# Kernel optimization log

Measured on AMD Instinct MI355X. Metric: run time of the kernel, lower is better.

The kernel has to match this reference:

```python
import jax, jax.numpy as jnp
import numpy as np

H = 1024   # dim_hidden
K = 64     # number of tasks
T_STEPS = 2048


def setup_inputs() -> dict:
    key = jax.random.key(0)
    ks = jax.random.split(key, 12)
    s = 1.0 / np.sqrt(H)
    inp = {
        "z":    jax.random.normal(ks[0], (H,), jnp.float32),
        "Wih":  jax.random.normal(ks[1], (4 * H, H), jnp.float32) * s,
        "Whh":  jax.random.normal(ks[2], (4 * H, H), jnp.float32) * s,
        "b_ih": jax.random.normal(ks[3], (4 * H,), jnp.float32) * s,
        "b_hh": jax.random.normal(ks[4], (4 * H,), jnp.float32) * s,
        "W1":   jax.random.normal(ks[5], (32, H), jnp.float32) * s,
        "b1":   jax.random.normal(ks[6], (32,), jnp.float32) * s,
        "W2":   jax.random.normal(ks[7], (32, 32), jnp.float32) * (1.0 / np.sqrt(32)),
        "b2":   jax.random.normal(ks[8], (32,), jnp.float32) * (1.0 / np.sqrt(32)),
        "W3":   jax.random.normal(ks[9], (K, 32), jnp.float32) * (1.0 / np.sqrt(32)),
        "b3":   jax.random.normal(ks[10], (K,), jnp.float32) * (1.0 / np.sqrt(32)),
        "T":    T_STEPS,
    }
    return inp


def reference(z, Wih, Whh, b_ih, b_hh, W1, b1, W2, b2, W3, b3, T):
    h0 = jnp.zeros_like(z)
    c0 = jnp.zeros_like(z)

    def cell(carry, _):
        x, h, c = carry  # x is the LSTM input this step (z first, then fed-back h)
        gates = x @ Wih.T + b_ih + h @ Whh.T + b_hh  # (4H,), torch gate order i,f,g,o
        i, f, g, o = jnp.split(gates, 4)
        c_new = jax.nn.sigmoid(f) * c + jax.nn.sigmoid(i) * jnp.tanh(g)
        h_new = jax.nn.sigmoid(o) * jnp.tanh(c_new)
        # torch LSTM output y == h_new; fed back as next input
        return (h_new, h_new, c_new), h_new

    _, hs = jax.lax.scan(cell, (z, h0, c0), None, length=T)  # hs: (T, H)

    # MLP applied per timestep, vectorized over T
    a = jax.nn.relu(hs @ W1.T + b1)
    a = jax.nn.relu(a @ W2.T + b2)
    rewards = a @ W3.T + b3  # (T, K)
    return rewards
```

## Files before the change

kernel.cpp:

```cpp
#include <hip/hip_runtime.h>
#include <math.h>

#define H        1024
#define TSTEPS   2048
#define NWG      64
#define NT       1024
#define PAD      68
#define SENT     0xFFFFFFFFu

typedef unsigned u32x4 __attribute__((ext_vector_type(4)));
typedef float    f32x2 __attribute__((ext_vector_type(2)));
typedef float    f32x4 __attribute__((ext_vector_type(4)));
typedef unsigned long long u64;

__device__ __forceinline__ u32x4 load16_agent(const unsigned* p) {
    u32x4 r;
    asm volatile("global_load_dwordx4 %0, %1, off sc1\n\ts_waitcnt vmcnt(0)"
                 : "=v"(r) : "v"(p) : "memory");
    return r;
}

__device__ __forceinline__ u64 load8_agent(const unsigned* p) {
    u64 r;
    asm volatile("global_load_dwordx2 %0, %1, off sc1\n\ts_waitcnt vmcnt(0)"
                 : "=v"(r) : "v"(p) : "memory");
    return r;
}

__device__ __forceinline__ void pkfma(f32x2& acc, f32x2 a, f32x2 b) {
    asm("v_pk_fma_f32 %0, %1, %2, %0" : "+v"(acc) : "v"(a), "v"(b));
}

__device__ __forceinline__ float fsig(float x)   { return 1.0f / (1.0f + __expf(-x)); }
__device__ __forceinline__ float ftanh_(float x) { return 1.0f - 2.0f / (__expf(2.0f * x) + 1.0f); }

__global__ __launch_bounds__(NT, 1) void lstm_persistent(
    const float* __restrict__ z,   const float* __restrict__ Wih,
    const float* __restrict__ Whh, const float* __restrict__ b_ih,
    const float* __restrict__ b_hh,
    const float* __restrict__ W1,  const float* __restrict__ b1,
    const float* __restrict__ W2,  const float* __restrict__ b2,
    const float* __restrict__ W3,  const float* __restrict__ b3,
    float* __restrict__ out, float* __restrict__ hs)
{
    __shared__ __align__(16) float hbuf[2][16 * PAD];
    __shared__ unsigned h_out[2][16];
    __shared__ __align__(16) float mlp_buf[4][16 * PAD];
    __shared__ float a1_lds[4][32];
    __shared__ float a2_lds[4][32];

    const int tid  = threadIdx.x;
    const int wg   = blockIdx.x;
    const int wave = tid >> 6;
    const int lane = tid & 63;
    const int g    = lane >> 4;
    const int seg  = lane & 15;
    const int E    = wg * 16 + wave;
    const int grow = g * H + E;
    const float bias = b_ih[grow] + b_hh[grow];

    if (tid < 32) h_out[tid >> 4][tid & 15] = SENT;

    if (tid < 256) {
        float4 zv = *(const float4*)(z + tid * 4);
        *(float4*)(&hbuf[0][(tid >> 4) * PAD + (tid & 15) * 4]) = zv;
    }
    __syncthreads();

    f32x4 wreg[16];
    float s0 = 0.f, s1 = 0.f, s2 = 0.f, s3 = 0.f;
    const float* wihp = Wih + (size_t)grow * H + seg * 64;
    const float* whhp = Whh + (size_t)grow * H + seg * 64;
#pragma unroll
    for (int k = 0; k < 16; ++k) {
        f32x4 a  = *(const f32x4*)(wihp + 4 * k);
        f32x4 b  = *(const f32x4*)(whhp + 4 * k);
        f32x4 zz = *(const f32x4*)(&hbuf[0][seg * PAD + 4 * k]);
        float d = a.x * zz.x + a.y * zz.y + a.z * zz.z + a.w * zz.w;
        if ((k & 3) == 0) s0 += d; else if ((k & 3) == 1) s1 += d;
        else if ((k & 3) == 2) s2 += d; else s3 += d;
        wreg[k] = a + b;
    }
    float c_reg;
    {
        float acc = (s0 + s1) + (s2 + s3);
        acc += __shfl_xor(acc, 1); acc += __shfl_xor(acc, 2);
        acc += __shfl_xor(acc, 4); acc += __shfl_xor(acc, 8);
        float val = acc + bias;
        float act = (g == 2) ? ftanh_(val) : fsig(val);
        float si = __shfl(act, 0), tg = __shfl(act, 32), so = __shfl(act, 48);
        c_reg = si * tg;
        float hn = so * ftanh_(c_reg);
        if (lane == 0) ((volatile unsigned*)h_out[0])[wave] = __float_as_uint(hn);
        if (wave == 15) {
            unsigned v;
            do { v = ((volatile unsigned*)h_out[0])[lane & 15]; } while (!__all(v != SENT));
            if (lane < 16) {
                __hip_atomic_store((unsigned*)hs + wg * 16 + lane, v,
                                   __ATOMIC_RELAXED, __HIP_MEMORY_SCOPE_AGENT);
                ((volatile unsigned*)h_out[0])[lane] = SENT;
                hbuf[1][(wg >> 2) * PAD + ((wg * 16) & 63) + lane] = __uint_as_float(v);
            }
        }
    }

    for (int t = 1; t < TSTEPS; ++t) {
        const int q = t & 1;
        if (tid < 512 && (tid >> 3) != wg) {
            const unsigned* p = (const unsigned*)hs + (size_t)(t - 1) * H + tid * 2;
            u64 a, b;
            asm volatile(
                "global_load_dwordx2 %0, %2, off sc1\n\t"
                "s_sleep 4\n\t"
                "global_load_dwordx2 %1, %2, off sc1\n\t"
                "1:\n\t"
                "s_waitcnt vmcnt(1)\n\t"
                "v_cmp_eq_u64 vcc, -1, %0\n\t"
                "s_cbranch_vccz 2f\n\t"
                "global_load_dwordx2 %0, %2, off sc1\n\t"
                "s_waitcnt vmcnt(1)\n\t"
                "v_cmp_eq_u64 vcc, -1, %1\n\t"
                "s_cbranch_vccz 2f\n\t"
                "global_load_dwordx2 %1, %2, off sc1\n\t"
                "s_branch 1b\n\t"
                "2:\n\t"
                "s_waitcnt vmcnt(0)"
                : "=&v"(a), "=&v"(b) : "v"(p) : "memory", "vcc");
            u64 sel = (((unsigned)a != SENT) && ((unsigned)(a >> 32) != SENT)) ? a : b;
            while (((unsigned)sel == SENT) || ((unsigned)(sel >> 32) == SENT))
                sel = load8_agent(p);
            const int e2 = tid * 2;
            float* dst = &hbuf[q][(e2 >> 6) * PAD + (e2 & 63)];
            dst[0] = __uint_as_float((unsigned)sel);
            dst[1] = __uint_as_float((unsigned)(sel >> 32));
        }
        __syncthreads();

        const float* hb = &hbuf[q][seg * PAD];
        f32x2 p0 = {0.f, 0.f}, p1 = {0.f, 0.f}, p2 = {0.f, 0.f}, p3 = {0.f, 0.f};
#pragma unroll
        for (int k = 0; k < 16; ++k) {
            f32x4 h4 = *(const f32x4*)(hb + 4 * k);
            f32x4 wv = wreg[k];
            if ((k & 1) == 0) { pkfma(p0, wv.xy, h4.xy); pkfma(p1, wv.zw, h4.zw); }
            else              { pkfma(p2, wv.xy, h4.xy); pkfma(p3, wv.zw, h4.zw); }
        }
        f32x2 ps = (p0 + p1) + (p2 + p3);
        float a2 = ps.x + ps.y;
        a2 += __shfl_xor(a2, 1); a2 += __shfl_xor(a2, 2);
        a2 += __shfl_xor(a2, 4); a2 += __shfl_xor(a2, 8);
        float val = a2 + bias;
        float act = (g == 2) ? ftanh_(val) : fsig(val);
        float si = __shfl(act, 0),  sf = __shfl(act, 16);
        float tg = __shfl(act, 32), so = __shfl(act, 48);
        float cn = sf * c_reg + si * tg;
        float hn = so * ftanh_(cn);
        c_reg = cn;
        if (lane == 0) ((volatile unsigned*)h_out[q])[wave] = __float_as_uint(hn);
        if (wave == 15) {
            unsigned v;
            do { v = ((volatile unsigned*)h_out[q])[lane & 15]; } while (!__all(v != SENT));
            if (lane < 16) {
                __hip_atomic_store((unsigned*)(hs + (size_t)t * H) + wg * 16 + lane, v,
                                   __ATOMIC_RELAXED, __HIP_MEMORY_SCOPE_AGENT);
                ((volatile unsigned*)h_out[q])[lane] = SENT;
                hbuf[q ^ 1][(wg >> 2) * PAD + ((wg * 16) & 63) + lane] =
                    __uint_as_float(v);
            }
        }
    }

    const int local = tid & 255;
    const int grp   = tid >> 8;
    const int row32 = local >> 3;
    const int sub   = local & 7;
    for (int ti = 0; ti < 8; ++ti) {
        int t = wg * 32 + ti * 4 + grp;
        __syncthreads();
        {
            const unsigned* p = (const unsigned*)hs + (size_t)t * H + local * 4;
            u32x4 v;
            for (;;) {
                v = load16_agent(p);
                if (v.x != SENT && v.y != SENT && v.z != SENT && v.w != SENT) break;
            }
            float* dst = &mlp_buf[grp][(local >> 4) * PAD + (local & 15) * 4];
            dst[0] = __uint_as_float(v.x); dst[1] = __uint_as_float(v.y);
            dst[2] = __uint_as_float(v.z); dst[3] = __uint_as_float(v.w);
        }
        __syncthreads();

        float acc1 = 0.f;
        const float* w1p = W1 + (size_t)row32 * H + sub * 128;
#pragma unroll
        for (int k = 0; k < 32; ++k) {
            float4 wv = *(const float4*)(w1p + 4 * k);
            int c = sub * 128 + 4 * k;
            float4 h4 = *(const float4*)(&mlp_buf[grp][(c >> 6) * PAD + (c & 63)]);
            acc1 += wv.x * h4.x + wv.y * h4.y + wv.z * h4.z + wv.w * h4.w;
        }
        acc1 += __shfl_xor(acc1, 1); acc1 += __shfl_xor(acc1, 2); acc1 += __shfl_xor(acc1, 4);
        if (sub == 0) a1_lds[grp][row32] = fmaxf(acc1 + b1[row32], 0.f);
        __syncthreads();

        if (local < 32) {
            float a = 0.f;
#pragma unroll
            for (int k = 0; k < 32; ++k) a += W2[local * 32 + k] * a1_lds[grp][k];
            a2_lds[grp][local] = fmaxf(a + b2[local], 0.f);
        }
        __syncthreads();

        if (local < 64) {
            float a = 0.f;
#pragma unroll
            for (int k = 0; k < 32; ++k) a += W3[local * 32 + k] * a2_lds[grp][k];
            out[(size_t)t * 64 + local] = a + b3[local];
        }
    }
}

extern "C" void kernel_launch(void* const* d_in, const int* in_sizes, int n_in,
                              void* d_out, int out_size, void* d_ws, size_t ws_size,
                              hipStream_t stream) {
    const float* z    = (const float*)d_in[0];
    const float* Wih  = (const float*)d_in[1];
    const float* Whh  = (const float*)d_in[2];
    const float* b_ih = (const float*)d_in[3];
    const float* b_hh = (const float*)d_in[4];
    const float* W1   = (const float*)d_in[5];
    const float* b1   = (const float*)d_in[6];
    const float* W2   = (const float*)d_in[7];
    const float* b2   = (const float*)d_in[8];
    const float* W3   = (const float*)d_in[9];
    const float* b3   = (const float*)d_in[10];
    float* out = (float*)d_out;

    float* hs = (float*)d_ws;

    hipMemsetAsync(hs, 0xFF, (size_t)TSTEPS * H * sizeof(float), stream);
    hipLaunchKernelGGL(lstm_persistent, dim3(NWG), dim3(NT), 0, stream,
                       z, Wih, Whh, b_ih, b_hh, W1, b1, W2, b2, W3, b3,
                       out, hs);
}
```

Before: 4.343 ms.

## Write polled hidden state to LDS in asm and add NaN-triggered fallback reload

The cross-workgroup polling loop now writes the selected 64-bit value straight to LDS inside the inline asm and exits without waiting for the outstanding second load. This drops the trailing vmcnt(0) wait and the follow-up C++ retry loop. Correctness is kept by a rare fallback: if the dot product comes out NaN, meaning a sentinel value slipped through, the wave reloads h from global memory with agent-scope loads and recomputes. The pre-load sleep is also lengthened. The risks are loads still in flight across iterations, since pa and pb are written late, and an extra NaN check on every step.

```diff
diff --git a/kernel.cpp b/kernel.cpp
--- a/kernel.cpp
+++ b/kernel.cpp
@@ -20,19 +20,16 @@
     return r;
 }
 
-__device__ __forceinline__ u64 load8_agent(const unsigned* p) {
-    u64 r;
-    asm volatile("global_load_dwordx2 %0, %1, off sc1\n\ts_waitcnt vmcnt(0)"
-                 : "=v"(r) : "v"(p) : "memory");
-    return r;
-}
-
 __device__ __forceinline__ void pkfma(f32x2& acc, f32x2 a, f32x2 b) {
     asm("v_pk_fma_f32 %0, %1, %2, %0" : "+v"(acc) : "v"(a), "v"(b));
 }
 
 __device__ __forceinline__ float fsig(float x)   { return 1.0f / (1.0f + __expf(-x)); }
 __device__ __forceinline__ float ftanh_(float x) { return 1.0f - 2.0f / (__expf(2.0f * x) + 1.0f); }
+
+__device__ __forceinline__ bool ok4(u32x4 v) {
+    return v.x != SENT && v.y != SENT && v.z != SENT && v.w != SENT;
+}
 
 __global__ __launch_bounds__(NT, 1) void lstm_persistent(
     const float* __restrict__ z,   const float* __restrict__ Wih,
@@ -104,14 +101,17 @@
         }
     }
 
+    u64 pa = 0, pb = 0;
+
     for (int t = 1; t < TSTEPS; ++t) {
         const int q = t & 1;
         if (tid < 512 && (tid >> 3) != wg) {
             const unsigned* p = (const unsigned*)hs + (size_t)(t - 1) * H + tid * 2;
-            u64 a, b;
+            const int e2 = tid * 2;
+            unsigned dst = (unsigned)(size_t)&hbuf[q][(e2 >> 6) * PAD + (e2 & 63)];
             asm volatile(
                 "global_load_dwordx2 %0, %2, off sc1\n\t"
-                "s_sleep 4\n\t"
+                "s_sleep 8\n\t"
                 "global_load_dwordx2 %1, %2, off sc1\n\t"
                 "1:\n\t"
                 "s_waitcnt vmcnt(1)\n\t"
@@ -120,19 +120,18 @@
                 "global_load_dwordx2 %0, %2, off sc1\n\t"
                 "s_waitcnt vmcnt(1)\n\t"
                 "v_cmp_eq_u64 vcc, -1, %1\n\t"
-                "s_cbranch_vccz 2f\n\t"
+                "s_cbranch_vccz 3f\n\t"
                 "global_load_dwordx2 %1, %2, off sc1\n\t"
                 "s_branch 1b\n\t"
                 "2:\n\t"
-                "s_waitcnt vmcnt(0)"
-                : "=&v"(a), "=&v"(b) : "v"(p) : "memory", "vcc");
-            u64 sel = (((unsigned)a != SENT) && ((unsigned)(a >> 32) != SENT)) ? a : b;
-            while (((unsigned)sel == SENT) || ((unsigned)(sel >> 32) == SENT))
-                sel = load8_agent(p);
-            const int e2 = tid * 2;
-            float* dst = &hbuf[q][(e2 >> 6) * PAD + (e2 & 63)];
-            dst[0] = __uint_as_float((unsigned)sel);
-            dst[1] = __uint_as_float((unsigned)(sel >> 32));
+                "ds_write_b64 %3, %0\n\t"
+                "s_branch 4f\n\t"
+                "3:\n\t"
+                "ds_write_b64 %3, %1\n\t"
+                "4:"
+                : "+v"(pa), "+v"(pb)
+                : "v"(p), "v"(dst)
+                : "memory", "vcc");
         }
         __syncthreads();
 
@@ -149,6 +148,26 @@
         float a2 = ps.x + ps.y;
         a2 += __shfl_xor(a2, 1); a2 += __shfl_xor(a2, 2);
         a2 += __shfl_xor(a2, 4); a2 += __shfl_xor(a2, 8);
+
+        if (__builtin_expect(__any(a2 != a2), 0)) {
+            const unsigned* pp = (const unsigned*)hs + (size_t)(t - 1) * H + seg * 64;
+            f32x2 r0 = {0.f,0.f}, r1 = {0.f,0.f}, r2 = {0.f,0.f}, r3 = {0.f,0.f};
+            for (int k = 0; k < 16; ++k) {
+                u32x4 v;
+                for (;;) { v = load16_agent(pp + 4 * k); if (ok4(v)) break; }
+                f32x4 h4;
+                h4.x = __uint_as_float(v.x); h4.y = __uint_as_float(v.y);
+                h4.z = __uint_as_float(v.z); h4.w = __uint_as_float(v.w);
+                f32x4 wv = wreg[k];
+                if ((k & 1) == 0) { pkfma(r0, wv.xy, h4.xy); pkfma(r1, wv.zw, h4.zw); }
+                else              { pkfma(r2, wv.xy, h4.xy); pkfma(r3, wv.zw, h4.zw); }
+            }
+            f32x2 rs = (r0 + r1) + (r2 + r3);
+            a2 = rs.x + rs.y;
+            a2 += __shfl_xor(a2, 1); a2 += __shfl_xor(a2, 2);
+            a2 += __shfl_xor(a2, 4); a2 += __shfl_xor(a2, 8);
+        }
+
         float val = a2 + bias;
         float act = (g == 2) ? ftanh_(val) : fsig(val);
         float si = __shfl(act, 0),  sf = __shfl(act, 16);
@@ -170,6 +189,8 @@
         }
     }
 
+    asm volatile("s_waitcnt vmcnt(0)" :: "v"(pa), "v"(pb) : "memory");
+
     const int local = tid & 255;
     const int grp   = tid >> 8;
     const int row32 = local >> 3;
@@ -182,7 +203,7 @@
             u32x4 v;
             for (;;) {
                 v = load16_agent(p);
-                if (v.x != SENT && v.y != SENT && v.z != SENT && v.w != SENT) break;
+                if (ok4(v)) break;
             }
             float* dst = &mlp_buf[grp][(local >> 4) * PAD + (local & 15) * 4];
             dst[0] = __uint_as_float(v.x); dst[1] = __uint_as_float(v.y);
```

New measurement: 4.268 ms. About the same (-1.7%).
